# Kernel optimization log

Hardware: AMD Instinct MI355X
Metric: run time of the kernel (lower is better)

Reference implementation:

```python
import jax, jax.numpy as jnp
import numpy as np

VOCAB, EMB, HID = 256, 32, 128
B, T = 512, 512


def setup_inputs() -> dict:
    key = jax.random.key(0)
    ks = jax.random.split(key, 8)
    s_emb = 1.0  # torch nn.Embedding default N(0,1)
    s_lstm = 1.0 / np.sqrt(HID)  # torch LSTM uniform(-1/sqrt(H), 1/sqrt(H))
    s_cls = 1.0 / np.sqrt(HID)
    return {
        "inputs": jax.random.randint(ks[0], (B, T), 0, VOCAB, dtype=jnp.int64),
        "emb": jax.random.normal(ks[1], (VOCAB, EMB), jnp.float32) * s_emb,
        "W_ih": jax.random.uniform(ks[2], (4 * HID, EMB), jnp.float32, -s_lstm, s_lstm),
        "W_hh": jax.random.uniform(ks[3], (4 * HID, HID), jnp.float32, -s_lstm, s_lstm),
        "b_ih": jax.random.uniform(ks[4], (4 * HID,), jnp.float32, -s_lstm, s_lstm),
        "b_hh": jax.random.uniform(ks[5], (4 * HID,), jnp.float32, -s_lstm, s_lstm),
        "W_cls": jax.random.uniform(ks[6], (VOCAB, HID), jnp.float32, -s_cls, s_cls),
        "b_cls": jax.random.uniform(ks[7], (VOCAB,), jnp.float32, -s_cls, s_cls),
    }


def reference(inputs, emb, W_ih, W_hh, b_ih, b_hh, W_cls, b_cls):
    x = emb[inputs]  # [B, T, E]
    H = W_hh.shape[1]
    # Precompute input projections for all timesteps (batched GEMM): [B, T, 4H]
    xw = jnp.einsum("bte,ge->btg", x, W_ih) + b_ih + b_hh
    xw_t = jnp.transpose(xw, (1, 0, 2))  # [T, B, 4H]

    def step(carry, xw_step):
        h, c = carry
        gates = xw_step + h @ W_hh.T  # [B, 4H]
        i, f, g, o = jnp.split(gates, 4, axis=-1)  # torch gate order: i, f, g, o
        i = jax.nn.sigmoid(i)
        f = jax.nn.sigmoid(f)
        g = jnp.tanh(g)
        o = jax.nn.sigmoid(o)
        c = f * c + i * g
        h = o * jnp.tanh(c)
        return (h, c), None

    h0 = jnp.zeros((x.shape[0], H), x.dtype)
    c0 = jnp.zeros((x.shape[0], H), x.dtype)
    (h_last, _), _ = jax.lax.scan(step, (h0, c0), xw_t)
    # classifier on last hidden state: [B, vocab]
    return h_last @ W_cls.T + b_cls
```

## Files before the change

kernel.cpp:

```cpp
#include <hip/hip_runtime.h>
#include <hip/hip_bf16.h>

#define VOCAB 256
#define EMB   32
#define HID   128
#define GATES 512
#define BATCH 512
#define SEQ   512
#define HSTRIDE 144

#define LOG2E 1.442695041f
#if __has_builtin(__builtin_amdgcn_exp2f)
#define GEXP(x) __builtin_amdgcn_exp2f(x)
#define SCALE_IFO LOG2E
#define SCALE_G   (2.0f * LOG2E)
#else
#define GEXP(x) __expf(x)
#define SCALE_IFO 1.0f
#define SCALE_G   2.0f
#endif

typedef __attribute__((ext_vector_type(8))) short bf16x8;
typedef __attribute__((ext_vector_type(4))) float f32x4;

static __device__ __forceinline__ unsigned short f2bf(float f) {
  unsigned int u = __float_as_uint(f);
  return (unsigned short)((u + 0x7fffu + ((u >> 16) & 1u)) >> 16);
}

__global__ __launch_bounds__(256) void prep_kernel(
    const float* __restrict__ emb, const float* __restrict__ W_ih,
    const float* __restrict__ W_hh, const float* __restrict__ b_ih,
    const float* __restrict__ b_hh, float* __restrict__ P,
    unsigned short* __restrict__ Whh_bf) {
  const int wg  = blockIdx.x;
  const int tid = threadIdx.x;
  if (wg < VOCAB) {
    __shared__ float e[EMB];
    if (tid < EMB) e[tid] = emb[wg * EMB + tid];
    __syncthreads();
    for (int g = tid; g < GATES; g += 256) {
      float acc = b_ih[g] + b_hh[g];
      const float* w = W_ih + g * EMB;
      #pragma unroll
      for (int k = 0; k < EMB; ++k) acc += e[k] * w[k];
      const float sc = ((g >> 7) == 2) ? SCALE_G : SCALE_IFO;
      P[wg * GATES + g] = acc * sc;
    }
  } else {
    const int base = (wg - VOCAB) * 1024 + tid * 4;
    const float sc = (((base >> 14) & 3) == 2) ? SCALE_G : SCALE_IFO;
    const float4 v = *(const float4*)(W_hh + base);
    ushort4 o;
    o.x = f2bf(v.x * sc); o.y = f2bf(v.y * sc);
    o.z = f2bf(v.z * sc); o.w = f2bf(v.w * sc);
    *(ushort4*)(Whh_bf + base) = o;
  }
}

__global__ __launch_bounds__(512, 2) void lstm_kernel(
    const int* __restrict__ inputs, const float* __restrict__ P,
    const unsigned short* __restrict__ Whh_bf,
    const float* __restrict__ W_cls, const float* __restrict__ b_cls,
    float* __restrict__ out) {
  const int wg   = blockIdx.x;
  const int tid  = threadIdx.x;
  const int wave = tid >> 6;
  const int lane = tid & 63;
  const int c16  = lane & 15;
  const int kg   = lane >> 4;
  const int b0   = wg * 4;

  const int row   = kg;
  const int jfull = wave * 16 + c16;

  __shared__ unsigned int   offs[SEQ][4];
  __shared__ unsigned short hbufA[4 * HSTRIDE];
  __shared__ unsigned short hbufB[4 * HSTRIDE];
  __shared__ float          h_last[4][HID];

  for (int k = tid; k < 4 * SEQ; k += 512) {
    const int r = k & 3, t = k >> 2;
    offs[t][r] = ((unsigned int)(inputs[(b0 + r) * SEQ + t] & 0xff)) << 9;
  }
  for (int k = tid; k < 4 * HSTRIDE; k += 512) { hbufA[k] = 0; hbufB[k] = 0; }

  bf16x8 Bfrag[4][4];
  #pragma unroll
  for (int gt = 0; gt < 4; ++gt) {
    const int g = gt * 128 + wave * 16 + c16;
    #pragma unroll
    for (int ks = 0; ks < 4; ++ks)
      Bfrag[gt][ks] = *(const bf16x8*)(Whh_bf + g * HID + ks * 32 + kg * 8);
  }

  const int aoff = (c16 & 3) * HSTRIDE + kg * 8;
  float cstate = 0.f;
  float hv = 0.f;

  __syncthreads();

  f32x4 pcur[4];
  {
    const uint4 o4 = *(const uint4*)&offs[0][0];
    const float* r0 = P + o4.x + jfull;
    const float* r1 = P + o4.y + jfull;
    const float* r2 = P + o4.z + jfull;
    const float* r3 = P + o4.w + jfull;
    #pragma unroll
    for (int gt = 0; gt < 4; ++gt) {
      pcur[gt][0] = r0[gt * 128]; pcur[gt][1] = r1[gt * 128];
      pcur[gt][2] = r2[gt * 128]; pcur[gt][3] = r3[gt * 128];
    }
  }

#define STEP(HIN, HOUT, T)                                                     \
  {                                                                            \
                     \
    const uint4 o4 = *(const uint4*)&offs[((T) + 1) & (SEQ - 1)][0];           \
    f32x4 pn0, pn1, pn2, pn3;                                                  \
    {                                                                          \
      const float* r0 = P + o4.x + jfull;                                      \
      const float* r1 = P + o4.y + jfull;                                      \
      const float* r2 = P + o4.z + jfull;                                      \
      const float* r3 = P + o4.w + jfull;                                      \
      pn0[0] = r0[0];   pn0[1] = r1[0];   pn0[2] = r2[0];   pn0[3] = r3[0];    \
      pn1[0] = r0[128]; pn1[1] = r1[128]; pn1[2] = r2[128]; pn1[3] = r3[128];  \
      pn2[0] = r0[256]; pn2[1] = r1[256]; pn2[2] = r2[256]; pn2[3] = r3[256];  \
      pn3[0] = r0[384]; pn3[1] = r1[384]; pn3[2] = r2[384]; pn3[3] = r3[384];  \
    }                                                                          \
    const unsigned short* hb = (HIN) + aoff;                                   \
    const bf16x8 A0 = *(const bf16x8*)(hb);                                    \
    const bf16x8 A1 = *(const bf16x8*)(hb + 32);                               \
    const bf16x8 A2 = *(const bf16x8*)(hb + 64);                               \
    const bf16x8 A3 = *(const bf16x8*)(hb + 96);                               \
    f32x4 a0 = pcur[0], a1 = pcur[1], a2 = pcur[2], a3 = pcur[3];              \
    a0 = __builtin_amdgcn_mfma_f32_16x16x32_bf16(A0, Bfrag[0][0], a0, 0,0,0);  \
    a1 = __builtin_amdgcn_mfma_f32_16x16x32_bf16(A0, Bfrag[1][0], a1, 0,0,0);  \
    a2 = __builtin_amdgcn_mfma_f32_16x16x32_bf16(A0, Bfrag[2][0], a2, 0,0,0);  \
    a3 = __builtin_amdgcn_mfma_f32_16x16x32_bf16(A0, Bfrag[3][0], a3, 0,0,0);  \
    a0 = __builtin_amdgcn_mfma_f32_16x16x32_bf16(A1, Bfrag[0][1], a0, 0,0,0);  \
    a1 = __builtin_amdgcn_mfma_f32_16x16x32_bf16(A1, Bfrag[1][1], a1, 0,0,0);  \
    a2 = __builtin_amdgcn_mfma_f32_16x16x32_bf16(A1, Bfrag[2][1], a2, 0,0,0);  \
    a3 = __builtin_amdgcn_mfma_f32_16x16x32_bf16(A1, Bfrag[3][1], a3, 0,0,0);  \
    a0 = __builtin_amdgcn_mfma_f32_16x16x32_bf16(A2, Bfrag[0][2], a0, 0,0,0);  \
    a1 = __builtin_amdgcn_mfma_f32_16x16x32_bf16(A2, Bfrag[1][2], a1, 0,0,0);  \
    a2 = __builtin_amdgcn_mfma_f32_16x16x32_bf16(A2, Bfrag[2][2], a2, 0,0,0);  \
    a3 = __builtin_amdgcn_mfma_f32_16x16x32_bf16(A2, Bfrag[3][2], a3, 0,0,0);  \
    a0 = __builtin_amdgcn_mfma_f32_16x16x32_bf16(A3, Bfrag[0][3], a0, 0,0,0);  \
    a1 = __builtin_amdgcn_mfma_f32_16x16x32_bf16(A3, Bfrag[1][3], a1, 0,0,0);  \
    a2 = __builtin_amdgcn_mfma_f32_16x16x32_bf16(A3, Bfrag[2][3], a2, 0,0,0);  \
    a3 = __builtin_amdgcn_mfma_f32_16x16x32_bf16(A3, Bfrag[3][3], a3, 0,0,0);  \
    const float gi = (kg & 2) ? ((kg & 1) ? a0[3] : a0[2])                     \
                              : ((kg & 1) ? a0[1] : a0[0]);                    \
    const float gf = (kg & 2) ? ((kg & 1) ? a1[3] : a1[2])                     \
                              : ((kg & 1) ? a1[1] : a1[0]);                    \
    const float gg = (kg & 2) ? ((kg & 1) ? a2[3] : a2[2])                     \
                              : ((kg & 1) ? a2[1] : a2[0]);                    \
    const float go = (kg & 2) ? ((kg & 1) ? a3[3] : a3[2])                     \
                              : ((kg & 1) ? a3[1] : a3[0]);                    \
    const float iv = __builtin_amdgcn_rcpf(1.f + GEXP(-gi));                   \
    const float fv = __builtin_amdgcn_rcpf(1.f + GEXP(-gf));                   \
    const float gv = 1.f - 2.f * __builtin_amdgcn_rcpf(GEXP(gg) + 1.f);        \
    const float ov = __builtin_amdgcn_rcpf(1.f + GEXP(-go));                   \
    cstate = fv * cstate + iv * gv;                                            \
    const float th =                                                           \
        1.f - 2.f * __builtin_amdgcn_rcpf(GEXP(cstate * SCALE_G) + 1.f);       \
    hv = ov * th;                                                              \
    (HOUT)[row * HSTRIDE + jfull] = f2bf(hv);                                  \
    pcur[0] = pn0; pcur[1] = pn1; pcur[2] = pn2; pcur[3] = pn3;                \
    __syncthreads();                                                           \
  }

  #pragma unroll 1
  for (int t = 0; t < SEQ; t += 2) {
    STEP(hbufA, hbufB, t)
    STEP(hbufB, hbufA, t + 1)
  }
#undef STEP

  h_last[row][jfull] = hv;
  __syncthreads();

  const int erow = tid >> 7;
  const int ej   = tid & 127;
  #pragma unroll
  for (int half = 0; half < 2; ++half) {
    const int v = ej + half * 128;
    float acc = b_cls[v];
    const float4* w  = (const float4*)(W_cls + v * HID);
    const float4* hh = (const float4*)&h_last[erow][0];
    #pragma unroll
    for (int k = 0; k < HID / 4; ++k) {
      const float4 wv = w[k];
      const float4 hv4 = hh[k];
      acc += wv.x * hv4.x + wv.y * hv4.y + wv.z * hv4.z + wv.w * hv4.w;
    }
    out[(b0 + erow) * VOCAB + v] = acc;
  }
}

extern "C" void kernel_launch(void* const* d_in, const int* in_sizes, int n_in,
                              void* d_out, int out_size, void* d_ws, size_t ws_size,
                              hipStream_t stream) {
  const int*   inputs = (const int*)d_in[0];
  const float* emb    = (const float*)d_in[1];
  const float* W_ih   = (const float*)d_in[2];
  const float* W_hh   = (const float*)d_in[3];
  const float* b_ih   = (const float*)d_in[4];
  const float* b_hh   = (const float*)d_in[5];
  const float* W_cls  = (const float*)d_in[6];
  const float* b_cls  = (const float*)d_in[7];
  float* outp = (float*)d_out;

  float* Ptab = (float*)d_ws;
  unsigned short* Whh_bf = (unsigned short*)((char*)d_ws + VOCAB * GATES * sizeof(float));

  prep_kernel<<<VOCAB + 64, 256, 0, stream>>>(emb, W_ih, W_hh, b_ih, b_hh, Ptab, Whh_bf);
  lstm_kernel<<<BATCH / 4, 512, 0, stream>>>(inputs, Ptab, Whh_bf, W_cls, b_cls, outp);
}
```

Measured before the change: 369.1 us.

## Gather per-lane input projections post-MFMA and convert W_hh to bf16 in-kernel

Result: faster. 314.4 us (-14.8%).

```diff
diff --git a/kernel.cpp b/kernel.cpp
--- a/kernel.cpp
+++ b/kernel.cpp
@@ -30,37 +30,26 @@
 
 __global__ __launch_bounds__(256) void prep_kernel(
     const float* __restrict__ emb, const float* __restrict__ W_ih,
-    const float* __restrict__ W_hh, const float* __restrict__ b_ih,
-    const float* __restrict__ b_hh, float* __restrict__ P,
-    unsigned short* __restrict__ Whh_bf) {
+    const float* __restrict__ b_ih, const float* __restrict__ b_hh,
+    float* __restrict__ P) {
   const int wg  = blockIdx.x;
   const int tid = threadIdx.x;
-  if (wg < VOCAB) {
-    __shared__ float e[EMB];
-    if (tid < EMB) e[tid] = emb[wg * EMB + tid];
-    __syncthreads();
-    for (int g = tid; g < GATES; g += 256) {
-      float acc = b_ih[g] + b_hh[g];
-      const float* w = W_ih + g * EMB;
-      #pragma unroll
-      for (int k = 0; k < EMB; ++k) acc += e[k] * w[k];
-      const float sc = ((g >> 7) == 2) ? SCALE_G : SCALE_IFO;
-      P[wg * GATES + g] = acc * sc;
-    }
-  } else {
-    const int base = (wg - VOCAB) * 1024 + tid * 4;
-    const float sc = (((base >> 14) & 3) == 2) ? SCALE_G : SCALE_IFO;
-    const float4 v = *(const float4*)(W_hh + base);
-    ushort4 o;
-    o.x = f2bf(v.x * sc); o.y = f2bf(v.y * sc);
-    o.z = f2bf(v.z * sc); o.w = f2bf(v.w * sc);
-    *(ushort4*)(Whh_bf + base) = o;
+  __shared__ float e[EMB];
+  if (tid < EMB) e[tid] = emb[wg * EMB + tid];
+  __syncthreads();
+  for (int g = tid; g < GATES; g += 256) {
+    float acc = b_ih[g] + b_hh[g];
+    const float* w = W_ih + g * EMB;
+    #pragma unroll
+    for (int k = 0; k < EMB; ++k) acc += e[k] * w[k];
+    const float sc = ((g >> 7) == 2) ? SCALE_G : SCALE_IFO;
+    P[wg * GATES + g] = acc * sc;
   }
 }
 
 __global__ __launch_bounds__(512, 2) void lstm_kernel(
     const int* __restrict__ inputs, const float* __restrict__ P,
-    const unsigned short* __restrict__ Whh_bf,
+    const float* __restrict__ W_hh,
     const float* __restrict__ W_cls, const float* __restrict__ b_cls,
     float* __restrict__ out) {
   const int wg   = blockIdx.x;
@@ -74,67 +63,57 @@
   const int row   = kg;
   const int jfull = wave * 16 + c16;
 
-  __shared__ unsigned int   offs[SEQ][4];
+  __shared__ unsigned char  chars[4][SEQ];
   __shared__ unsigned short hbufA[4 * HSTRIDE];
   __shared__ unsigned short hbufB[4 * HSTRIDE];
   __shared__ float          h_last[4][HID];
 
   for (int k = tid; k < 4 * SEQ; k += 512) {
-    const int r = k & 3, t = k >> 2;
-    offs[t][r] = ((unsigned int)(inputs[(b0 + r) * SEQ + t] & 0xff)) << 9;
+    const int r = k >> 9, t = k & (SEQ - 1);
+    chars[r][t] = (unsigned char)(inputs[(b0 + r) * SEQ + t] & 0xff);
   }
   for (int k = tid; k < 4 * HSTRIDE; k += 512) { hbufA[k] = 0; hbufB[k] = 0; }
 
   bf16x8 Bfrag[4][4];
   #pragma unroll
   for (int gt = 0; gt < 4; ++gt) {
-    const int g = gt * 128 + wave * 16 + c16;
+    const float sc = (gt == 2) ? SCALE_G : SCALE_IFO;
+    const float* wr = W_hh + (gt * 128 + wave * 16 + c16) * HID + kg * 8;
     #pragma unroll
-    for (int ks = 0; ks < 4; ++ks)
-      Bfrag[gt][ks] = *(const bf16x8*)(Whh_bf + g * HID + ks * 32 + kg * 8);
+    for (int ks = 0; ks < 4; ++ks) {
+      const float4 w0 = *(const float4*)(wr + ks * 32);
+      const float4 w1 = *(const float4*)(wr + ks * 32 + 4);
+      bf16x8 b;
+      b[0] = (short)f2bf(w0.x * sc); b[1] = (short)f2bf(w0.y * sc);
+      b[2] = (short)f2bf(w0.z * sc); b[3] = (short)f2bf(w0.w * sc);
+      b[4] = (short)f2bf(w1.x * sc); b[5] = (short)f2bf(w1.y * sc);
+      b[6] = (short)f2bf(w1.z * sc); b[7] = (short)f2bf(w1.w * sc);
+      Bfrag[gt][ks] = b;
+    }
   }
 
   const int aoff = (c16 & 3) * HSTRIDE + kg * 8;
+  const float* Pj = P + jfull;
   float cstate = 0.f;
   float hv = 0.f;
 
   __syncthreads();
 
-  f32x4 pcur[4];
-  {
-    const uint4 o4 = *(const uint4*)&offs[0][0];
-    const float* r0 = P + o4.x + jfull;
-    const float* r1 = P + o4.y + jfull;
-    const float* r2 = P + o4.z + jfull;
-    const float* r3 = P + o4.w + jfull;
-    #pragma unroll
-    for (int gt = 0; gt < 4; ++gt) {
-      pcur[gt][0] = r0[gt * 128]; pcur[gt][1] = r1[gt * 128];
-      pcur[gt][2] = r2[gt * 128]; pcur[gt][3] = r3[gt * 128];
-    }
-  }
+  const float* Pr0 = Pj + ((size_t)chars[row][0] << 9);
+  float p0 = Pr0[0], p1 = Pr0[128], p2 = Pr0[256], p3 = Pr0[384];
 
 #define STEP(HIN, HOUT, T)                                                     \
   {                                                                            \
-                     \
-    const uint4 o4 = *(const uint4*)&offs[((T) + 1) & (SEQ - 1)][0];           \
-    f32x4 pn0, pn1, pn2, pn3;                                                  \
-    {                                                                          \
-      const float* r0 = P + o4.x + jfull;                                      \
-      const float* r1 = P + o4.y + jfull;                                      \
-      const float* r2 = P + o4.z + jfull;                                      \
-      const float* r3 = P + o4.w + jfull;                                      \
-      pn0[0] = r0[0];   pn0[1] = r1[0];   pn0[2] = r2[0];   pn0[3] = r3[0];    \
-      pn1[0] = r0[128]; pn1[1] = r1[128]; pn1[2] = r2[128]; pn1[3] = r3[128];  \
-      pn2[0] = r0[256]; pn2[1] = r1[256]; pn2[2] = r2[256]; pn2[3] = r3[256];  \
-      pn3[0] = r0[384]; pn3[1] = r1[384]; pn3[2] = r2[384]; pn3[3] = r3[384];  \
-    }                                                                          \
+           \
+    const int chn = chars[row][((T) + 1) & (SEQ - 1)];                         \
+    const float* Pn = Pj + ((size_t)chn << 9);                                 \
+    const float q0 = Pn[0], q1 = Pn[128], q2 = Pn[256], q3 = Pn[384];          \
     const unsigned short* hb = (HIN) + aoff;                                   \
     const bf16x8 A0 = *(const bf16x8*)(hb);                                    \
     const bf16x8 A1 = *(const bf16x8*)(hb + 32);                               \
     const bf16x8 A2 = *(const bf16x8*)(hb + 64);                               \
     const bf16x8 A3 = *(const bf16x8*)(hb + 96);                               \
-    f32x4 a0 = pcur[0], a1 = pcur[1], a2 = pcur[2], a3 = pcur[3];              \
+    f32x4 a0 = {}, a1 = {}, a2 = {}, a3 = {};                                  \
     a0 = __builtin_amdgcn_mfma_f32_16x16x32_bf16(A0, Bfrag[0][0], a0, 0,0,0);  \
     a1 = __builtin_amdgcn_mfma_f32_16x16x32_bf16(A0, Bfrag[1][0], a1, 0,0,0);  \
     a2 = __builtin_amdgcn_mfma_f32_16x16x32_bf16(A0, Bfrag[2][0], a2, 0,0,0);  \
@@ -159,16 +138,16 @@
                               : ((kg & 1) ? a2[1] : a2[0]);                    \
     const float go = (kg & 2) ? ((kg & 1) ? a3[3] : a3[2])                     \
                               : ((kg & 1) ? a3[1] : a3[0]);                    \
-    const float iv = __builtin_amdgcn_rcpf(1.f + GEXP(-gi));                   \
-    const float fv = __builtin_amdgcn_rcpf(1.f + GEXP(-gf));                   \
-    const float gv = 1.f - 2.f * __builtin_amdgcn_rcpf(GEXP(gg) + 1.f);        \
-    const float ov = __builtin_amdgcn_rcpf(1.f + GEXP(-go));                   \
+    const float iv = __builtin_amdgcn_rcpf(1.f + GEXP(-(gi + p0)));            \
+    const float fv = __builtin_amdgcn_rcpf(1.f + GEXP(-(gf + p1)));            \
+    const float gv = 1.f - 2.f * __builtin_amdgcn_rcpf(GEXP(gg + p2) + 1.f);   \
+    const float ov = __builtin_amdgcn_rcpf(1.f + GEXP(-(go + p3)));            \
     cstate = fv * cstate + iv * gv;                                            \
     const float th =                                                           \
         1.f - 2.f * __builtin_amdgcn_rcpf(GEXP(cstate * SCALE_G) + 1.f);       \
     hv = ov * th;                                                              \
     (HOUT)[row * HSTRIDE + jfull] = f2bf(hv);                                  \
-    pcur[0] = pn0; pcur[1] = pn1; pcur[2] = pn2; pcur[3] = pn3;                \
+    p0 = q0; p1 = q1; p2 = q2; p3 = q3;                                        \
     __syncthreads();                                                           \
   }
 
@@ -214,8 +193,7 @@
   float* outp = (float*)d_out;
 
   float* Ptab = (float*)d_ws;
-  unsigned short* Whh_bf = (unsigned short*)((char*)d_ws + VOCAB * GATES * sizeof(float));
 
-  prep_kernel<<<VOCAB + 64, 256, 0, stream>>>(emb, W_ih, W_hh, b_ih, b_hh, Ptab, Whh_bf);
-  lstm_kernel<<<BATCH / 4, 512, 0, stream>>>(inputs, Ptab, Whh_bf, W_cls, b_cls, outp);
+  prep_kernel<<<VOCAB, 256, 0, stream>>>(emb, W_ih, b_ih, b_hh, Ptab);
+  lstm_kernel<<<BATCH / 4, 512, 0, stream>>>(inputs, Ptab, W_hh, W_cls, b_cls, outp);
 }
```
